# Kernel tuning notes

Hardware: AMD Instinct MI355X
Metric: run time of the kernel (lower is better)

The kernel has to match this reference:

```python
import jax, jax.numpy as jnp
import numpy as np
from jax import lax

B, S, I, H, L = 128, 256, 64, 128, 64
N_SUB = 2  # fixed RK4 substeps per observation interval (replaces adaptive dopri5)


def setup_inputs() -> dict:
    key = jax.random.key(0)
    ks = jax.random.split(key, 16)
    sc = 0.05
    x = jax.random.normal(ks[0], (B, S, I), jnp.float32)
    # strictly increasing irregular observation times
    times = jnp.sort(jax.random.uniform(ks[1], (S,), jnp.float32) * 10.0)
    return {
        "x": x,
        "times": times,
        "W_ih": jax.random.normal(ks[2], (3 * H, I), jnp.float32) * sc,
        "W_hh": jax.random.normal(ks[3], (3 * H, H), jnp.float32) * sc,
        "b_ih": jnp.zeros((3 * H,), jnp.float32),
        "b_hh": jnp.zeros((3 * H,), jnp.float32),
        "ode_W1": jax.random.normal(ks[4], (H, H), jnp.float32) * sc,
        "ode_b1": jnp.zeros((H,), jnp.float32),
        "ode_W2": jax.random.normal(ks[5], (H, H), jnp.float32) * sc,
        "ode_b2": jnp.zeros((H,), jnp.float32),
        "W_mean": jax.random.normal(ks[6], (L, H), jnp.float32) * sc,
        "b_mean": jnp.zeros((L,), jnp.float32),
        "W_logvar": jax.random.normal(ks[7], (L, H), jnp.float32) * sc,
        "b_logvar": jnp.zeros((L,), jnp.float32),
    }


def reference(x, times, W_ih, W_hh, b_ih, b_hh, ode_W1, ode_b1, ode_W2, ode_b2,
              W_mean, b_mean, W_logvar, b_logvar):
    def ode_f(h):  # MLP dynamics: Linear -> tanh -> Linear (time-independent)
        return jnp.tanh(h @ ode_W1.T + ode_b1) @ ode_W2.T + ode_b2

    def rk4(h, dt):
        k1 = ode_f(h)
        k2 = ode_f(h + 0.5 * dt * k1)
        k3 = ode_f(h + 0.5 * dt * k2)
        k4 = ode_f(h + dt * k3)
        return h + (dt / 6.0) * (k1 + 2.0 * k2 + 2.0 * k3 + k4)

    def gru(x_t, h):  # torch.nn.GRUCell math
        gx = x_t @ W_ih.T + b_ih
        gh = h @ W_hh.T + b_hh
        rx, zx, nx = jnp.split(gx, 3, axis=-1)
        rh, zh, nh = jnp.split(gh, 3, axis=-1)
        r = jax.nn.sigmoid(rx + rh)
        z = jax.nn.sigmoid(zx + zh)
        n = jnp.tanh(nx + r * nh)
        return (1.0 - z) * n + z * h

    # iterate i = S-1 .. 0; before each GRU update (except the first, i=S-1)
    # evolve h from t_{i+1} backward to t_i  -> dt_i = t_i - t_{i+1} (negative)
    dt_rev = jnp.concatenate([jnp.zeros((1,), times.dtype),
                              (times[:-1] - times[1:])[::-1]])  # [S]
    x_rev = jnp.transpose(x[:, ::-1, :], (1, 0, 2))  # [S, B, I]

    def step(h, inp):
        x_t, dt = inp
        sub = dt / N_SUB
        for _ in range(N_SUB):  # fixed small unroll
            h = rk4(h, sub)
        h = gru(x_t, h)
        return h, None

    h0 = jnp.zeros((x.shape[0], W_hh.shape[1]), x.dtype)
    h, _ = lax.scan(step, h0, (x_rev, dt_rev))
    mean = h @ W_mean.T + b_mean
    logvar = h @ W_logvar.T + b_logvar
    return (mean, logvar)
```

## Files before the change

kernel.cpp:

```cpp
#include <hip/hip_runtime.h>

#define NB 128
#define NS 256
#define NI 64
#define NH 128
#define NL 64
#define NG 384

typedef _Float16 f16;
typedef __attribute__((ext_vector_type(2))) _Float16 f16x2;

__device__ __forceinline__ float fast_tanh(float x) {
    float e = __expf(2.0f * x);
    return 1.0f - 2.0f / (e + 1.0f);
}
__device__ __forceinline__ float fast_sig(float x) {
    return 1.0f / (1.0f + __expf(-x));
}
template <int CTRL>
__device__ __forceinline__ float dpp_xor_add(float a) {
    int ai = __builtin_bit_cast(int, a);
    int bi = __builtin_amdgcn_update_dpp(0, ai, CTRL, 0xF, 0xF, true);
    return a + __builtin_bit_cast(float, bi);
}
__device__ __forceinline__ float quad_red(float a) {
    a = dpp_xor_add<0xB1>(a);
    a = dpp_xor_add<0x4E>(a);
    return a;
}
__device__ __forceinline__ float fdot2(f16x2 a, f16x2 b, float c) {
#if __has_builtin(__builtin_amdgcn_fdot2)
    return __builtin_amdgcn_fdot2(a, b, c, false);
#else
    return c + (float)a.x * (float)b.x + (float)a.y * (float)b.y;
#endif
}
__device__ __forceinline__ f16x2 bc16(unsigned int u) {
    return __builtin_bit_cast(f16x2, u);
}
__device__ __forceinline__ void sync_lds() {
    asm volatile("s_waitcnt lgkmcnt(0)" ::: "memory");
    __builtin_amdgcn_s_barrier();
    asm volatile("" ::: "memory");
}

__device__ __align__(16) f16 g_W1h[NH * NH];
__device__ __align__(16) f16 g_W2h[NH * NH];
__device__ __align__(16) f16 g_W12h[NH * NH];
__device__ __align__(16) f16 g_Whhh[3 * NH * NH];
__device__ __align__(16) f16 g_Whh2h[3 * NH * NH];
__device__ float g_w1b2[NH];
__device__ float g_whhb2[3 * NH];

__global__ __launch_bounds__(384)
void gx_kernel(const float* __restrict__ x, const float* __restrict__ W_ih,
               const float* __restrict__ b_ih, float* __restrict__ gx)
{
    const int s = blockIdx.x;
    const int j = threadIdx.x;
    __shared__ __align__(16) float xs[NB * NI];
    for (int idx = j; idx < NB * NI; idx += 384) {
        int bb = idx >> 6, cc = idx & 63;
        xs[idx] = x[(bb * NS + s) * NI + cc];
    }
    float w[64];
#pragma unroll
    for (int c = 0; c < 64; c += 4)
        *(float4*)&w[c] = *(const float4*)&W_ih[j * NI + c];
    const float bj = b_ih[j];
    __syncthreads();
    for (int bb = 0; bb < NB; bb++) {
        const float* xr = xs + bb * NI;
        float a0 = 0.f, a1 = 0.f, a2 = 0.f, a3 = 0.f;
#pragma unroll
        for (int c = 0; c < 64; c += 4) {
            a0 = fmaf(w[c + 0], xr[c + 0], a0);
            a1 = fmaf(w[c + 1], xr[c + 1], a1);
            a2 = fmaf(w[c + 2], xr[c + 2], a2);
            a3 = fmaf(w[c + 3], xr[c + 3], a3);
        }
        gx[((size_t)s * NB + bb) * NG + j] = ((a0 + a1) + (a2 + a3)) + bj;
    }
}

__global__ __launch_bounds__(128)
void prep_kernel(const float* __restrict__ W1, const float* __restrict__ Whh,
                 const float* __restrict__ W2, const float* __restrict__ b2)
{
    const int i = blockIdx.x;
    const int j = threadIdx.x;
    __shared__ float rowA[NH];
    __shared__ float red[NH];
    const float* src = (i < NH) ? (W1 + i * NH) : (Whh + (size_t)(i - NH) * NH);
    rowA[j] = src[j];
    __syncthreads();
    float acc = 0.f;
    for (int k = 0; k < NH; k++) acc = fmaf(rowA[k], W2[k * NH + j], acc);
    if (i < NH) {
        g_W12h[i * NH + j] = (f16)acc;
        g_W1h[i * NH + j]  = (f16)rowA[j];
        g_W2h[i * NH + j]  = (f16)W2[i * NH + j];
    } else {
        g_Whh2h[(size_t)(i - NH) * NH + j] = (f16)acc;
        g_Whhh[(size_t)(i - NH) * NH + j]  = (f16)rowA[j];
    }
    red[j] = rowA[j] * b2[j];
    __syncthreads();
    for (int off = 64; off > 0; off >>= 1) {
        if (j < off) red[j] += red[j + off];
        __syncthreads();
    }
    if (j == 0) {
        if (i < NH) g_w1b2[i] = red[0];
        else        g_whhb2[i - NH] = red[0];
    }
}

#define CHNK(SRC, OB) (*(const uint4*)((const unsigned char*)(SRC) + (OB)))

#define D4(W, K, V, A0, A1, A2, A3)                                            \
    A0 = fdot2(W[K + 0], bc16((V).x), A0);                                     \
    A1 = fdot2(W[K + 1], bc16((V).y), A1);                                     \
    A2 = fdot2(W[K + 2], bc16((V).z), A2);                                     \
    A3 = fdot2(W[K + 3], bc16((V).w), A3);

#define D2(W, K, V, A0, A1)                                                    \
    A0 = fdot2(W[K + 0], bc16((V).x), A0);                                     \
    A1 = fdot2(W[K + 1], bc16((V).y), A1);                                     \
    A0 = fdot2(W[K + 2], bc16((V).z), A0);                                     \
    A1 = fdot2(W[K + 3], bc16((V).w), A1);

#define DOT1(W, SRC, OUT)                                                      \
    {                                                                          \
        float a0_ = 0.f, a1_ = 0.f, a2_ = 0.f, a3_ = 0.f;                      \
        { uint4 v_ = CHNK(SRC, ob0); D4(W, 0,  v_, a0_, a1_, a2_, a3_) }       \
        { uint4 v_ = CHNK(SRC, ob1); D4(W, 4,  v_, a0_, a1_, a2_, a3_) }       \
        { uint4 v_ = CHNK(SRC, ob2); D4(W, 8,  v_, a0_, a1_, a2_, a3_) }       \
        { uint4 v_ = CHNK(SRC, ob3); D4(W, 12, v_, a0_, a1_, a2_, a3_) }       \
        OUT = quad_red((a0_ + a1_) + (a2_ + a3_));                             \
    }

#define DOT2S(WA, WB, SRC, OA, OB)                                             \
    {                                                                          \
        float a0_ = 0.f, a1_ = 0.f, a2_ = 0.f, a3_ = 0.f;                      \
        float b0_ = 0.f, b1_ = 0.f, b2_ = 0.f, b3_ = 0.f;                      \
        { uint4 v_ = CHNK(SRC, ob0); D4(WA, 0,  v_, a0_, a1_, a2_, a3_) D4(WB, 0,  v_, b0_, b1_, b2_, b3_) } \
        { uint4 v_ = CHNK(SRC, ob1); D4(WA, 4,  v_, a0_, a1_, a2_, a3_) D4(WB, 4,  v_, b0_, b1_, b2_, b3_) } \
        { uint4 v_ = CHNK(SRC, ob2); D4(WA, 8,  v_, a0_, a1_, a2_, a3_) D4(WB, 8,  v_, b0_, b1_, b2_, b3_) } \
        { uint4 v_ = CHNK(SRC, ob3); D4(WA, 12, v_, a0_, a1_, a2_, a3_) D4(WB, 12, v_, b0_, b1_, b2_, b3_) } \
        OA = quad_red((a0_ + a1_) + (a2_ + a3_));                              \
        OB = quad_red((b0_ + b1_) + (b2_ + b3_));                              \
    }

#define DOT2D(WA, SA, WB, SB, OA, OB)                                          \
    {                                                                          \
        float a0_ = 0.f, a1_ = 0.f, a2_ = 0.f, a3_ = 0.f;                      \
        float b0_ = 0.f, b1_ = 0.f, b2_ = 0.f, b3_ = 0.f;                      \
        { uint4 v_ = CHNK(SA, ob0); uint4 u_ = CHNK(SB, ob0); D4(WA, 0,  v_, a0_, a1_, a2_, a3_) D4(WB, 0,  u_, b0_, b1_, b2_, b3_) } \
        { uint4 v_ = CHNK(SA, ob1); uint4 u_ = CHNK(SB, ob1); D4(WA, 4,  v_, a0_, a1_, a2_, a3_) D4(WB, 4,  u_, b0_, b1_, b2_, b3_) } \
        { uint4 v_ = CHNK(SA, ob2); uint4 u_ = CHNK(SB, ob2); D4(WA, 8,  v_, a0_, a1_, a2_, a3_) D4(WB, 8,  u_, b0_, b1_, b2_, b3_) } \
        { uint4 v_ = CHNK(SA, ob3); uint4 u_ = CHNK(SB, ob3); D4(WA, 12, v_, a0_, a1_, a2_, a3_) D4(WB, 12, u_, b0_, b1_, b2_, b3_) } \
        OA = quad_red((a0_ + a1_) + (a2_ + a3_));                              \
        OB = quad_red((b0_ + b1_) + (b2_ + b3_));                              \
    }

#define DOT4S(WA, WB, WC, WD, SRC, OA, OB, OC, OD)                             \
    {                                                                          \
        float a0_ = 0.f, a1_ = 0.f, b0_ = 0.f, b1_ = 0.f;                      \
        float c0_ = 0.f, c1_ = 0.f, d0_ = 0.f, d1_ = 0.f;                      \
        { uint4 v_ = CHNK(SRC, ob0); D2(WA, 0,  v_, a0_, a1_) D2(WB, 0,  v_, b0_, b1_) D2(WC, 0,  v_, c0_, c1_) D2(WD, 0,  v_, d0_, d1_) } \
        { uint4 v_ = CHNK(SRC, ob1); D2(WA, 4,  v_, a0_, a1_) D2(WB, 4,  v_, b0_, b1_) D2(WC, 4,  v_, c0_, c1_) D2(WD, 4,  v_, d0_, d1_) } \
        { uint4 v_ = CHNK(SRC, ob2); D2(WA, 8,  v_, a0_, a1_) D2(WB, 8,  v_, b0_, b1_) D2(WC, 8,  v_, c0_, c1_) D2(WD, 8,  v_, d0_, d1_) } \
        { uint4 v_ = CHNK(SRC, ob3); D2(WA, 12, v_, a0_, a1_) D2(WB, 12, v_, b0_, b1_) D2(WC, 12, v_, c0_, c1_) D2(WD, 12, v_, d0_, d1_) } \
        OA = quad_red(a0_ + a1_);                                              \
        OB = quad_red(b0_ + b1_);                                              \
        OC = quad_red(c0_ + c1_);                                              \
        OD = quad_red(d0_ + d1_);                                              \
    }

#define LDCH(DST, K, BP, OB)                                                   \
    {                                                                          \
        uint4 v_ = *(const uint4*)((BP) + (OB));                               \
        DST[K + 0] = bc16(v_.x); DST[K + 1] = bc16(v_.y);                      \
        DST[K + 2] = bc16(v_.z); DST[K + 3] = bc16(v_.w);                      \
    }

#define LOADW(DST, BASE)                                                       \
    {                                                                          \
        const unsigned char* bp_ = (const unsigned char*)(BASE);               \
        LDCH(DST, 0, bp_, ob0) LDCH(DST, 4, bp_, ob1)                          \
        LDCH(DST, 8, bp_, ob2) LDCH(DST, 12, bp_, ob3)                         \
    }

__global__ __launch_bounds__(512, 2)
void rnn_kernel(const float* __restrict__ times, const float* __restrict__ b_hh,
                const float* __restrict__ b1, const float* __restrict__ b2,
                const float* __restrict__ W_mean, const float* __restrict__ b_mean,
                const float* __restrict__ W_logvar, const float* __restrict__ b_logvar,
                const float* __restrict__ gx,
                const float* __restrict__ x, const float* __restrict__ W_ih,
                const float* __restrict__ b_ih,
                const int use_gx,
                float* __restrict__ out)
{
    const int b = blockIdx.x;
    const int t = threadIdx.x;
    const int r = t >> 2;
    const int p = t & 3;

    __shared__ __align__(16) f16 shHh[NH], shUh[NH], shAh[NH];
    __shared__ float shT[NS];
    __shared__ __align__(16) float shGX[NG], shX[NI], shHf[NH];

    const int ob0 = 64 * p + 16 * ((0 + p) & 3);
    const int ob1 = 64 * p + 16 * ((1 + p) & 3);
    const int ob2 = 64 * p + 16 * ((2 + p) & 3);
    const int ob3 = 64 * p + 16 * ((3 + p) & 3);

    f16x2 w1p[16], w2p[16], w12p[16];
    f16x2 wh0p[16], wh1p[16], wh2p[16];
    f16x2 ws0p[16], ws1p[16], ws2p[16];
    LOADW(w1p,  g_W1h  + r * NH);
    LOADW(w2p,  g_W2h  + r * NH);
    LOADW(w12p, g_W12h + r * NH);
    LOADW(wh0p, g_Whhh + (0 * NH + r) * NH);
    LOADW(wh1p, g_Whhh + (1 * NH + r) * NH);
    LOADW(wh2p, g_Whhh + (2 * NH + r) * NH);
    LOADW(ws0p, g_Whh2h + (size_t)(0 * NH + r) * NH);
    LOADW(ws1p, g_Whh2h + (size_t)(1 * NH + r) * NH);
    LOADW(ws2p, g_Whh2h + (size_t)(2 * NH + r) * NH);

    const float b1r = b1[r], b2r = b2[r];
    const float bh0 = b_hh[r], bh1 = b_hh[NH + r], bh2 = b_hh[2 * NH + r];
    const float w1b2r = g_w1b2[r];
    const float wb0 = g_whhb2[r], wb1 = g_whhb2[NH + r], wb2 = g_whhb2[2 * NH + r];

    if (t < NS) shT[t] = times[t];
    if (t < NH) shHh[t] = (f16)0.f;
    float h = 0.f;
    __syncthreads();

    float gxr = 0.f, gxz = 0.f, gxn = 0.f;
    if (use_gx) {
        const float* g = gx + ((size_t)(NS - 1) * NB + b) * NG;
        gxr = g[r]; gxz = g[NH + r]; gxn = g[2 * NH + r];
    }

    for (int si = 0; si < NS; ++si) {
        const int seq = NS - 1 - si;
        const float dt = (si == 0) ? 0.f : (shT[seq] - shT[seq + 1]);
        const float dts = 0.5f * dt;
        const float a2 = 0.5f * dts;
        const float a6 = dts * (1.f / 6.f);

        float gnr = 0.f, gnz = 0.f, gnn = 0.f;
        if (use_gx) {
            const int seqn = (seq > 0) ? (seq - 1) : 0;
            const float* g = gx + ((size_t)seqn * NB + b) * NG;
            gnr = g[r]; gnz = g[NH + r]; gnn = g[2 * NH + r];
        } else {
            if (t < NI) shX[t] = x[(b * NS + seq) * NI + t];
            __syncthreads();
            if (t < NG) {
                const float* wr = W_ih + t * NI;
                float a = 0.f;
#pragma unroll
                for (int cc = 0; cc < NI; cc += 4) {
                    float4 w4 = *(const float4*)(wr + cc);
                    a = fmaf(w4.x, shX[cc + 0], a);
                    a = fmaf(w4.y, shX[cc + 1], a);
                    a = fmaf(w4.z, shX[cc + 2], a);
                    a = fmaf(w4.w, shX[cc + 3], a);
                }
                shGX[t] = a + b_ih[t];
            }
            __syncthreads();
        }

        float z1a, u, S, m;
        DOT1(w1p, shHh, z1a);
        z1a += b1r;
        u = fast_tanh(z1a);
        S = u;
        if (p == 0) shUh[r] = (f16)u;
        sync_lds();
        DOT1(w12p, shUh, m);
        u = fast_tanh(z1a + a2 * (m + w1b2r));
        S += 2.f * u;
        if (p == 0) shUh[r] = (f16)u;
        sync_lds();
        DOT1(w12p, shUh, m);
        u = fast_tanh(z1a + a2 * (m + w1b2r));
        S += 2.f * u;
        if (p == 0) shUh[r] = (f16)u;
        sync_lds();
        DOT1(w12p, shUh, m);
        u = fast_tanh(z1a + dts * (m + w1b2r));
        S += u;
        if (p == 0) shUh[r] = (f16)S;
        sync_lds();
        float mA, mB;
        DOT2S(w2p, w12p, shUh, mA, mB);
        const float hA = h + a6 * mA + dts * b2r;
        const float z1b = z1a + a6 * mB + dts * w1b2r;
        u = fast_tanh(z1b);
        float S2 = u;
        if (p == 0) { shAh[r] = (f16)hA; shUh[r] = (f16)u; }
        sync_lds();

        float g0, g1, g2;
        DOT2D(w12p, shUh, wh0p, shAh, m, g0);
        u = fast_tanh(z1b + a2 * (m + w1b2r));
        S2 += 2.f * u;
        if (p == 0) shUh[r] = (f16)u;
        sync_lds();
        DOT2D(w12p, shUh, wh1p, shAh, m, g1);
        u = fast_tanh(z1b + a2 * (m + w1b2r));
        S2 += 2.f * u;
        if (p == 0) shUh[r] = (f16)u;
        sync_lds();
        DOT2D(w12p, shUh, wh2p, shAh, m, g2);
        u = fast_tanh(z1b + dts * (m + w1b2r));
        S2 += u;
        if (p == 0) shUh[r] = (f16)S2;
        sync_lds();
        float n0, n1, n2, n3;
        DOT4S(w2p, ws0p, ws1p, ws2p, shUh, n0, n1, n2, n3);
        const float hB = hA + a6 * n0 + dts * b2r;
        const float rh = g0 + a6 * n1 + dts * wb0 + bh0;
        const float zh = g1 + a6 * n2 + dts * wb1 + bh1;
        const float nh = g2 + a6 * n3 + dts * wb2 + bh2;
        float rx, zx, nx;
        if (use_gx) { rx = gxr; zx = gxz; nx = gxn; }
        else        { rx = shGX[r]; zx = shGX[NH + r]; nx = shGX[2 * NH + r]; }
        const float rr = fast_sig(rx + rh);
        const float zz = fast_sig(zx + zh);
        const float nn = fast_tanh(nx + rr * nh);
        h = (1.f - zz) * nn + zz * hB;
        if (p == 0) shHh[r] = (f16)h;
        gxr = gnr; gxz = gnz; gxn = gnn;
        sync_lds();
    }

    if (p == 0) shHf[r] = h;
    __syncthreads();
    const int sel = r >> 6;
    const int l = r & 63;
    const float* Wf = sel ? W_logvar : W_mean;
    const int c0 = 32 * p;
    float a0 = 0.f, a1 = 0.f;
#pragma unroll
    for (int jj = 0; jj < 8; jj++) {
        float4 w4 = *(const float4*)&Wf[l * NH + c0 + 4 * jj];
        float4 h4 = *(const float4*)(shHf + c0 + 4 * jj);
        a0 = fmaf(w4.x, h4.x, a0);
        a1 = fmaf(w4.y, h4.y, a1);
        a0 = fmaf(w4.z, h4.z, a0);
        a1 = fmaf(w4.w, h4.w, a1);
    }
    float acc = quad_red(a0 + a1);
    if (p == 0) {
        const float bias = sel ? b_logvar[l] : b_mean[l];
        out[sel * (NB * NL) + b * NL + l] = acc + bias;
    }
}

extern "C" void kernel_launch(void* const* d_in, const int* in_sizes, int n_in,
                              void* d_out, int out_size, void* d_ws, size_t ws_size,
                              hipStream_t stream)
{
    const float* x        = (const float*)d_in[0];
    const float* times    = (const float*)d_in[1];
    const float* W_ih     = (const float*)d_in[2];
    const float* W_hh     = (const float*)d_in[3];
    const float* b_ih     = (const float*)d_in[4];
    const float* b_hh     = (const float*)d_in[5];
    const float* W1       = (const float*)d_in[6];
    const float* b1       = (const float*)d_in[7];
    const float* W2       = (const float*)d_in[8];
    const float* b2       = (const float*)d_in[9];
    const float* W_mean   = (const float*)d_in[10];
    const float* b_mean   = (const float*)d_in[11];
    const float* W_logvar = (const float*)d_in[12];
    const float* b_logvar = (const float*)d_in[13];
    float* out = (float*)d_out;

    float* gxbuf = (float*)d_ws;
    const size_t need = (size_t)NS * NB * NG * sizeof(float);
    const int use_gx = (d_ws != nullptr && ws_size >= need) ? 1 : 0;

    if (use_gx) {
        gx_kernel<<<NS, 384, 0, stream>>>(x, W_ih, b_ih, gxbuf);
    }
    prep_kernel<<<512, 128, 0, stream>>>(W1, W_hh, W2, b2);
    rnn_kernel<<<NB, 512, 0, stream>>>(times, b_hh, b1, b2,
                                       W_mean, b_mean, W_logvar, b_logvar,
                                       gxbuf, x, W_ih, b_ih, use_gx, out);
}
```

Measured before the change: 912.1 us.

## Split each hidden row across two lanes instead of four in RNN kernel

Reduces the recurrent kernel from 512 to 256 threads per block, with each pair of lanes covering one hidden row over 64 elements and holding twice as many register-resident fp16 weights. Cross-lane reduction drops to a single DPP step, and the bank-rotated chunk offsets give way to contiguous loads. This cuts barrier participants and reduction work per serial step. The cost is much higher register pressure (288 f16x2 weight registers) and a longer dot-product chain per lane, which risks spills or lower latency hiding.

```diff
diff --git a/kernel.cpp b/kernel.cpp
--- a/kernel.cpp
+++ b/kernel.cpp
@@ -17,16 +17,10 @@
 __device__ __forceinline__ float fast_sig(float x) {
     return 1.0f / (1.0f + __expf(-x));
 }
-template <int CTRL>
-__device__ __forceinline__ float dpp_xor_add(float a) {
+__device__ __forceinline__ float red1(float a) {
     int ai = __builtin_bit_cast(int, a);
-    int bi = __builtin_amdgcn_update_dpp(0, ai, CTRL, 0xF, 0xF, true);
+    int bi = __builtin_amdgcn_update_dpp(0, ai, 0xB1, 0xF, 0xF, true);
     return a + __builtin_bit_cast(float, bi);
-}
-__device__ __forceinline__ float quad_red(float a) {
-    a = dpp_xor_add<0xB1>(a);
-    a = dpp_xor_add<0x4E>(a);
-    return a;
 }
 __device__ __forceinline__ float fdot2(f16x2 a, f16x2 b, float c) {
 #if __has_builtin(__builtin_amdgcn_fdot2)
@@ -116,83 +110,102 @@
     }
 }
 
-#define CHNK(SRC, OB) (*(const uint4*)((const unsigned char*)(SRC) + (OB)))
-
-#define D4(W, K, V, A0, A1, A2, A3)                                            \
-    A0 = fdot2(W[K + 0], bc16((V).x), A0);                                     \
-    A1 = fdot2(W[K + 1], bc16((V).y), A1);                                     \
-    A2 = fdot2(W[K + 2], bc16((V).z), A2);                                     \
-    A3 = fdot2(W[K + 3], bc16((V).w), A3);
-
-#define D2(W, K, V, A0, A1)                                                    \
-    A0 = fdot2(W[K + 0], bc16((V).x), A0);                                     \
-    A1 = fdot2(W[K + 1], bc16((V).y), A1);                                     \
-    A0 = fdot2(W[K + 2], bc16((V).z), A0);                                     \
-    A1 = fdot2(W[K + 3], bc16((V).w), A1);
-
 #define DOT1(W, SRC, OUT)                                                      \
     {                                                                          \
         float a0_ = 0.f, a1_ = 0.f, a2_ = 0.f, a3_ = 0.f;                      \
-        { uint4 v_ = CHNK(SRC, ob0); D4(W, 0,  v_, a0_, a1_, a2_, a3_) }       \
-        { uint4 v_ = CHNK(SRC, ob1); D4(W, 4,  v_, a0_, a1_, a2_, a3_) }       \
-        { uint4 v_ = CHNK(SRC, ob2); D4(W, 8,  v_, a0_, a1_, a2_, a3_) }       \
-        { uint4 v_ = CHNK(SRC, ob3); D4(W, 12, v_, a0_, a1_, a2_, a3_) }       \
-        OUT = quad_red((a0_ + a1_) + (a2_ + a3_));                             \
+        _Pragma("unroll") for (int j = 0; j < 8; j++)                          \
+        {                                                                      \
+            uint4 v_ = *(const uint4*)((const unsigned char*)(SRC) + pbase + 16 * j); \
+            a0_ = fdot2(W[4 * j + 0], bc16(v_.x), a0_);                        \
+            a1_ = fdot2(W[4 * j + 1], bc16(v_.y), a1_);                        \
+            a2_ = fdot2(W[4 * j + 2], bc16(v_.z), a2_);                        \
+            a3_ = fdot2(W[4 * j + 3], bc16(v_.w), a3_);                        \
+        }                                                                      \
+        OUT = red1((a0_ + a1_) + (a2_ + a3_));                                 \
     }
 
 #define DOT2S(WA, WB, SRC, OA, OB)                                             \
     {                                                                          \
         float a0_ = 0.f, a1_ = 0.f, a2_ = 0.f, a3_ = 0.f;                      \
         float b0_ = 0.f, b1_ = 0.f, b2_ = 0.f, b3_ = 0.f;                      \
-        { uint4 v_ = CHNK(SRC, ob0); D4(WA, 0,  v_, a0_, a1_, a2_, a3_) D4(WB, 0,  v_, b0_, b1_, b2_, b3_) } \
-        { uint4 v_ = CHNK(SRC, ob1); D4(WA, 4,  v_, a0_, a1_, a2_, a3_) D4(WB, 4,  v_, b0_, b1_, b2_, b3_) } \
-        { uint4 v_ = CHNK(SRC, ob2); D4(WA, 8,  v_, a0_, a1_, a2_, a3_) D4(WB, 8,  v_, b0_, b1_, b2_, b3_) } \
-        { uint4 v_ = CHNK(SRC, ob3); D4(WA, 12, v_, a0_, a1_, a2_, a3_) D4(WB, 12, v_, b0_, b1_, b2_, b3_) } \
-        OA = quad_red((a0_ + a1_) + (a2_ + a3_));                              \
-        OB = quad_red((b0_ + b1_) + (b2_ + b3_));                              \
+        _Pragma("unroll") for (int j = 0; j < 8; j++)                          \
+        {                                                                      \
+            uint4 v_ = *(const uint4*)((const unsigned char*)(SRC) + pbase + 16 * j); \
+            a0_ = fdot2(WA[4 * j + 0], bc16(v_.x), a0_);                       \
+            a1_ = fdot2(WA[4 * j + 1], bc16(v_.y), a1_);                       \
+            a2_ = fdot2(WA[4 * j + 2], bc16(v_.z), a2_);                       \
+            a3_ = fdot2(WA[4 * j + 3], bc16(v_.w), a3_);                       \
+            b0_ = fdot2(WB[4 * j + 0], bc16(v_.x), b0_);                       \
+            b1_ = fdot2(WB[4 * j + 1], bc16(v_.y), b1_);                       \
+            b2_ = fdot2(WB[4 * j + 2], bc16(v_.z), b2_);                       \
+            b3_ = fdot2(WB[4 * j + 3], bc16(v_.w), b3_);                       \
+        }                                                                      \
+        OA = red1((a0_ + a1_) + (a2_ + a3_));                                  \
+        OB = red1((b0_ + b1_) + (b2_ + b3_));                                  \
     }
 
 #define DOT2D(WA, SA, WB, SB, OA, OB)                                          \
     {                                                                          \
         float a0_ = 0.f, a1_ = 0.f, a2_ = 0.f, a3_ = 0.f;                      \
         float b0_ = 0.f, b1_ = 0.f, b2_ = 0.f, b3_ = 0.f;                      \
-        { uint4 v_ = CHNK(SA, ob0); uint4 u_ = CHNK(SB, ob0); D4(WA, 0,  v_, a0_, a1_, a2_, a3_) D4(WB, 0,  u_, b0_, b1_, b2_, b3_) } \
-        { uint4 v_ = CHNK(SA, ob1); uint4 u_ = CHNK(SB, ob1); D4(WA, 4,  v_, a0_, a1_, a2_, a3_) D4(WB, 4,  u_, b0_, b1_, b2_, b3_) } \
-        { uint4 v_ = CHNK(SA, ob2); uint4 u_ = CHNK(SB, ob2); D4(WA, 8,  v_, a0_, a1_, a2_, a3_) D4(WB, 8,  u_, b0_, b1_, b2_, b3_) } \
-        { uint4 v_ = CHNK(SA, ob3); uint4 u_ = CHNK(SB, ob3); D4(WA, 12, v_, a0_, a1_, a2_, a3_) D4(WB, 12, u_, b0_, b1_, b2_, b3_) } \
-        OA = quad_red((a0_ + a1_) + (a2_ + a3_));                              \
-        OB = quad_red((b0_ + b1_) + (b2_ + b3_));                              \
+        _Pragma("unroll") for (int j = 0; j < 8; j++)                          \
+        {                                                                      \
+            uint4 v_ = *(const uint4*)((const unsigned char*)(SA) + pbase + 16 * j); \
+            uint4 u_ = *(const uint4*)((const unsigned char*)(SB) + pbase + 16 * j); \
+            a0_ = fdot2(WA[4 * j + 0], bc16(v_.x), a0_);                       \
+            a1_ = fdot2(WA[4 * j + 1], bc16(v_.y), a1_);                       \
+            a2_ = fdot2(WA[4 * j + 2], bc16(v_.z), a2_);                       \
+            a3_ = fdot2(WA[4 * j + 3], bc16(v_.w), a3_);                       \
+            b0_ = fdot2(WB[4 * j + 0], bc16(u_.x), b0_);                       \
+            b1_ = fdot2(WB[4 * j + 1], bc16(u_.y), b1_);                       \
+            b2_ = fdot2(WB[4 * j + 2], bc16(u_.z), b2_);                       \
+            b3_ = fdot2(WB[4 * j + 3], bc16(u_.w), b3_);                       \
+        }                                                                      \
+        OA = red1((a0_ + a1_) + (a2_ + a3_));                                  \
+        OB = red1((b0_ + b1_) + (b2_ + b3_));                                  \
     }
 
 #define DOT4S(WA, WB, WC, WD, SRC, OA, OB, OC, OD)                             \
     {                                                                          \
         float a0_ = 0.f, a1_ = 0.f, b0_ = 0.f, b1_ = 0.f;                      \
         float c0_ = 0.f, c1_ = 0.f, d0_ = 0.f, d1_ = 0.f;                      \
-        { uint4 v_ = CHNK(SRC, ob0); D2(WA, 0,  v_, a0_, a1_) D2(WB, 0,  v_, b0_, b1_) D2(WC, 0,  v_, c0_, c1_) D2(WD, 0,  v_, d0_, d1_) } \
-        { uint4 v_ = CHNK(SRC, ob1); D2(WA, 4,  v_, a0_, a1_) D2(WB, 4,  v_, b0_, b1_) D2(WC, 4,  v_, c0_, c1_) D2(WD, 4,  v_, d0_, d1_) } \
-        { uint4 v_ = CHNK(SRC, ob2); D2(WA, 8,  v_, a0_, a1_) D2(WB, 8,  v_, b0_, b1_) D2(WC, 8,  v_, c0_, c1_) D2(WD, 8,  v_, d0_, d1_) } \
-        { uint4 v_ = CHNK(SRC, ob3); D2(WA, 12, v_, a0_, a1_) D2(WB, 12, v_, b0_, b1_) D2(WC, 12, v_, c0_, c1_) D2(WD, 12, v_, d0_, d1_) } \
-        OA = quad_red(a0_ + a1_);                                              \
-        OB = quad_red(b0_ + b1_);                                              \
-        OC = quad_red(c0_ + c1_);                                              \
-        OD = quad_red(d0_ + d1_);                                              \
-    }
-
-#define LDCH(DST, K, BP, OB)                                                   \
-    {                                                                          \
-        uint4 v_ = *(const uint4*)((BP) + (OB));                               \
-        DST[K + 0] = bc16(v_.x); DST[K + 1] = bc16(v_.y);                      \
-        DST[K + 2] = bc16(v_.z); DST[K + 3] = bc16(v_.w);                      \
+        _Pragma("unroll") for (int j = 0; j < 8; j++)                          \
+        {                                                                      \
+            uint4 v_ = *(const uint4*)((const unsigned char*)(SRC) + pbase + 16 * j); \
+            a0_ = fdot2(WA[4 * j + 0], bc16(v_.x), a0_);                       \
+            a1_ = fdot2(WA[4 * j + 1], bc16(v_.y), a1_);                       \
+            a0_ = fdot2(WA[4 * j + 2], bc16(v_.z), a0_);                       \
+            a1_ = fdot2(WA[4 * j + 3], bc16(v_.w), a1_);                       \
+            b0_ = fdot2(WB[4 * j + 0], bc16(v_.x), b0_);                       \
+            b1_ = fdot2(WB[4 * j + 1], bc16(v_.y), b1_);                       \
+            b0_ = fdot2(WB[4 * j + 2], bc16(v_.z), b0_);                       \
+            b1_ = fdot2(WB[4 * j + 3], bc16(v_.w), b1_);                       \
+            c0_ = fdot2(WC[4 * j + 0], bc16(v_.x), c0_);                       \
+            c1_ = fdot2(WC[4 * j + 1], bc16(v_.y), c1_);                       \
+            c0_ = fdot2(WC[4 * j + 2], bc16(v_.z), c0_);                       \
+            c1_ = fdot2(WC[4 * j + 3], bc16(v_.w), c1_);                       \
+            d0_ = fdot2(WD[4 * j + 0], bc16(v_.x), d0_);                       \
+            d1_ = fdot2(WD[4 * j + 1], bc16(v_.y), d1_);                       \
+            d0_ = fdot2(WD[4 * j + 2], bc16(v_.z), d0_);                       \
+            d1_ = fdot2(WD[4 * j + 3], bc16(v_.w), d1_);                       \
+        }                                                                      \
+        OA = red1(a0_ + a1_);                                                  \
+        OB = red1(b0_ + b1_);                                                  \
+        OC = red1(c0_ + c1_);                                                  \
+        OD = red1(d0_ + d1_);                                                  \
     }
 
 #define LOADW(DST, BASE)                                                       \
     {                                                                          \
-        const unsigned char* bp_ = (const unsigned char*)(BASE);               \
-        LDCH(DST, 0, bp_, ob0) LDCH(DST, 4, bp_, ob1)                          \
-        LDCH(DST, 8, bp_, ob2) LDCH(DST, 12, bp_, ob3)                         \
-    }
-
-__global__ __launch_bounds__(512, 2)
+        _Pragma("unroll") for (int j = 0; j < 8; j++)                          \
+        {                                                                      \
+            uint4 v_ = *(const uint4*)((const unsigned char*)(BASE) + pbase + 16 * j); \
+            DST[4 * j + 0] = bc16(v_.x); DST[4 * j + 1] = bc16(v_.y);          \
+            DST[4 * j + 2] = bc16(v_.z); DST[4 * j + 3] = bc16(v_.w);          \
+        }                                                                      \
+    }
+
+__global__ __launch_bounds__(256, 1)
 void rnn_kernel(const float* __restrict__ times, const float* __restrict__ b_hh,
                 const float* __restrict__ b1, const float* __restrict__ b2,
                 const float* __restrict__ W_mean, const float* __restrict__ b_mean,
@@ -205,21 +218,17 @@
 {
     const int b = blockIdx.x;
     const int t = threadIdx.x;
-    const int r = t >> 2;
-    const int p = t & 3;
+    const int r = t >> 1;
+    const int p = t & 1;
+    const int pbase = 128 * p;
 
     __shared__ __align__(16) f16 shHh[NH], shUh[NH], shAh[NH];
     __shared__ float shT[NS];
     __shared__ __align__(16) float shGX[NG], shX[NI], shHf[NH];
 
-    const int ob0 = 64 * p + 16 * ((0 + p) & 3);
-    const int ob1 = 64 * p + 16 * ((1 + p) & 3);
-    const int ob2 = 64 * p + 16 * ((2 + p) & 3);
-    const int ob3 = 64 * p + 16 * ((3 + p) & 3);
-
-    f16x2 w1p[16], w2p[16], w12p[16];
-    f16x2 wh0p[16], wh1p[16], wh2p[16];
-    f16x2 ws0p[16], ws1p[16], ws2p[16];
+    f16x2 w1p[32], w2p[32], w12p[32];
+    f16x2 wh0p[32], wh1p[32], wh2p[32];
+    f16x2 ws0p[32], ws1p[32], ws2p[32];
     LOADW(w1p,  g_W1h  + r * NH);
     LOADW(w2p,  g_W2h  + r * NH);
     LOADW(w12p, g_W12h + r * NH);
@@ -261,8 +270,8 @@
         } else {
             if (t < NI) shX[t] = x[(b * NS + seq) * NI + t];
             __syncthreads();
-            if (t < NG) {
-                const float* wr = W_ih + t * NI;
+            for (int idx = t; idx < NG; idx += 256) {
+                const float* wr = W_ih + idx * NI;
                 float a = 0.f;
 #pragma unroll
                 for (int cc = 0; cc < NI; cc += 4) {
@@ -272,7 +281,7 @@
                     a = fmaf(w4.z, shX[cc + 2], a);
                     a = fmaf(w4.w, shX[cc + 3], a);
                 }
-                shGX[t] = a + b_ih[t];
+                shGX[idx] = a + b_ih[idx];
             }
             __syncthreads();
         }
@@ -281,18 +290,18 @@
         DOT1(w1p, shHh, z1a);
         z1a += b1r;
         u = fast_tanh(z1a);
+        if (p == 0) shUh[r] = (f16)u;
         S = u;
-        if (p == 0) shUh[r] = (f16)u;
         sync_lds();
         DOT1(w12p, shUh, m);
         u = fast_tanh(z1a + a2 * (m + w1b2r));
+        if (p == 0) shUh[r] = (f16)u;
         S += 2.f * u;
-        if (p == 0) shUh[r] = (f16)u;
         sync_lds();
         DOT1(w12p, shUh, m);
         u = fast_tanh(z1a + a2 * (m + w1b2r));
+        if (p == 0) shUh[r] = (f16)u;
         S += 2.f * u;
-        if (p == 0) shUh[r] = (f16)u;
         sync_lds();
         DOT1(w12p, shUh, m);
         u = fast_tanh(z1a + dts * (m + w1b2r));
@@ -304,20 +313,20 @@
         const float hA = h + a6 * mA + dts * b2r;
         const float z1b = z1a + a6 * mB + dts * w1b2r;
         u = fast_tanh(z1b);
+        if (p == 0) { shAh[r] = (f16)hA; shUh[r] = (f16)u; }
         float S2 = u;
-        if (p == 0) { shAh[r] = (f16)hA; shUh[r] = (f16)u; }
         sync_lds();
 
         float g0, g1, g2;
         DOT2D(w12p, shUh, wh0p, shAh, m, g0);
         u = fast_tanh(z1b + a2 * (m + w1b2r));
+        if (p == 0) shUh[r] = (f16)u;
         S2 += 2.f * u;
-        if (p == 0) shUh[r] = (f16)u;
         sync_lds();
         DOT2D(w12p, shUh, wh1p, shAh, m, g1);
         u = fast_tanh(z1b + a2 * (m + w1b2r));
+        if (p == 0) shUh[r] = (f16)u;
         S2 += 2.f * u;
-        if (p == 0) shUh[r] = (f16)u;
         sync_lds();
         DOT2D(w12p, shUh, wh2p, shAh, m, g2);
         u = fast_tanh(z1b + dts * (m + w1b2r));
@@ -347,18 +356,18 @@
     const int sel = r >> 6;
     const int l = r & 63;
     const float* Wf = sel ? W_logvar : W_mean;
-    const int c0 = 32 * p;
+    const int hc0 = 64 * p;
     float a0 = 0.f, a1 = 0.f;
 #pragma unroll
-    for (int jj = 0; jj < 8; jj++) {
-        float4 w4 = *(const float4*)&Wf[l * NH + c0 + 4 * jj];
-        float4 h4 = *(const float4*)(shHf + c0 + 4 * jj);
+    for (int jj = 0; jj < 16; jj++) {
+        float4 w4 = *(const float4*)&Wf[l * NH + hc0 + 4 * jj];
+        float4 h4 = *(const float4*)(shHf + hc0 + 4 * jj);
         a0 = fmaf(w4.x, h4.x, a0);
         a1 = fmaf(w4.y, h4.y, a1);
         a0 = fmaf(w4.z, h4.z, a0);
         a1 = fmaf(w4.w, h4.w, a1);
     }
-    float acc = quad_red(a0 + a1);
+    float acc = red1(a0 + a1);
     if (p == 0) {
         const float bias = sel ? b_logvar[l] : b_mean[l];
         out[sel * (NB * NL) + b * NL + l] = acc + bias;
@@ -393,7 +402,7 @@
         gx_kernel<<<NS, 384, 0, stream>>>(x, W_ih, b_ih, gxbuf);
     }
     prep_kernel<<<512, 128, 0, stream>>>(W1, W_hh, W2, b2);
-    rnn_kernel<<<NB, 512, 0, stream>>>(times, b_hh, b1, b2,
+    rnn_kernel<<<NB, 256, 0, stream>>>(times, b_hh, b1, b2,
                                        W_mean, b_mean, W_logvar, b_logvar,
                                        gxbuf, x, W_ih, b_ih, use_gx, out);
 }
```

New measurement: 917.8 us. No clear change (+0.6%).
